# Performance work log

Hardware: AMD Instinct MI355X
Metric: run time of the kernel (lower is better)

Reference implementation:

```python
import jax, jax.numpy as jnp
import numpy as np

SIZE = 512  # context size
T, D1, D2 = 32768, 512, 512
HID = int(SIZE * 1.5)  # 768, units of the 'context_linear' Dense


def setup_inputs() -> dict:
    key = jax.random.key(0)
    ks = jax.random.split(key, 8)
    din = D1 + D2
    return {
        "x1": jax.random.normal(ks[0], (T, D1), jnp.float32),
        "x2": jax.random.normal(ks[1], (T, D2), jnp.float32),
        "context0": jax.random.normal(ks[2], (1, SIZE), jnp.float32) * 0.1,  # tf.Variable init stddev=0.1
        "W_linear": jax.random.normal(ks[3], (din, HID), jnp.float32) * 0.02,
        "b_linear": jnp.zeros((HID,), jnp.float32),
        "W_embed": jax.random.normal(ks[4], (HID, SIZE), jnp.float32) * 0.02,
        "W_rate": jax.random.normal(ks[5], (SIZE, 1), jnp.float32) * 0.02,
        "W_forget": jax.random.normal(ks[6], (SIZE, SIZE), jnp.float32) * 0.02,
    }


def reference(x1, x2, context0, W_linear, b_linear, W_embed, W_rate, W_forget):
    # z = embed(linear(concat(inputs))) : Dense(1.5*size, linear) -> Dense(size, sigmoid, no bias)
    z = jnp.concatenate([x1, x2], axis=-1)                      # [T, D1+D2]
    z = jax.nn.sigmoid((z @ W_linear + b_linear) @ W_embed)     # [T, SIZE]
    # rate gate depends only on z_t, so precompute it in one GEMM
    r = jnp.tanh(z @ W_rate)[:, 0]                              # [T]

    # recurrence: c_t = softmax(c_{t-1} @ Wf) * c_{t-1} + r_t * z_t
    def step(c, zr):
        zt, rt = zr
        f = jax.nn.softmax(c @ W_forget)                        # [SIZE]
        c_new = f * c + rt * zt
        return c_new, c_new

    _, ys = jax.lax.scan(step, context0[0], (z, r))             # ys: [T, SIZE]
    return ys
```

## Files before the change

### kernel.cpp

```cpp
#include <hip/hip_runtime.h>
#include <stdint.h>
#include <stddef.h>


typedef __attribute__((ext_vector_type(8))) short bf16x8;
typedef __attribute__((ext_vector_type(4))) float f32x4;

__device__ __forceinline__ unsigned short f32_to_bf16(float f) {
  union { float f; unsigned u; } v; v.f = f;
  unsigned u = v.u;
  return (unsigned short)((u + 0x7fffu + ((u >> 16) & 1u)) >> 16);
}

__device__ __forceinline__ unsigned char f32_to_e4m3(float f) {
  float a = fabsf(f);
  unsigned char s = (unsigned char)((__float_as_uint(f) >> 24) & 0x80u);
  if (a >= 448.0f) return s | 0x7Eu;
  if (a < 0.015625f) {
    unsigned m = (unsigned)rintf(a * 512.0f);
    return s | (unsigned char)m;
  }
  unsigned u = __float_as_uint(a);
  unsigned r = u + 0x7FFFFu + ((u >> 20) & 1u);
  unsigned e = (r >> 23) - 120u;
  unsigned m = (r >> 20) & 7u;
  if (e >= 16u) return s | 0x7Eu;
  return s | (unsigned char)((e << 3) | m);
}

__device__ __forceinline__ void pack_fp8x8(const float* c, unsigned char* dst) {
  int lo = 0, hi = 0;
  lo = __builtin_amdgcn_cvt_pk_fp8_f32(c[0] * 16.f, c[1] * 16.f, lo, false);
  lo = __builtin_amdgcn_cvt_pk_fp8_f32(c[2] * 16.f, c[3] * 16.f, lo, true);
  hi = __builtin_amdgcn_cvt_pk_fp8_f32(c[4] * 16.f, c[5] * 16.f, hi, false);
  hi = __builtin_amdgcn_cvt_pk_fp8_f32(c[6] * 16.f, c[7] * 16.f, hi, true);
  int2 v; v.x = lo; v.y = hi;
  *(int2*)dst = v;
}

__device__ __forceinline__ void async16(const void* g, void* l) {
  __builtin_amdgcn_global_load_lds(
      (const __attribute__((address_space(1))) unsigned int*)g,
      (__attribute__((address_space(3))) unsigned int*)l, 16, 0, 0);
}

__global__ void k_prep(const float* __restrict__ x1, const float* __restrict__ x2,
                       const float* __restrict__ Wl, const float* __restrict__ We,
                       const float* __restrict__ Wf,
                       unsigned short* __restrict__ Xb,
                       unsigned short* __restrict__ WlT,
                       unsigned short* __restrict__ WeT,
                       unsigned char* __restrict__ Wf8,
                       float* __restrict__ rb) {
  __shared__ float tile[32][33];
  int b = blockIdx.x;
  if (b >= 1440) {
    int id = (b - 1440) * 256 + threadIdx.x;
    int t  = id >> 8;
    int c4 = (id & 255) * 4;
    float4 v;
    if (c4 < 512) v = *(const float4*)(x1 + (size_t)t * 512 + c4);
    else          v = *(const float4*)(x2 + (size_t)t * 512 + (c4 - 512));
    ushort4 o;
    o.x = f32_to_bf16(v.x); o.y = f32_to_bf16(v.y);
    o.z = f32_to_bf16(v.z); o.w = f32_to_bf16(v.w);
    *(ushort4*)(Xb + (size_t)t * 1024 + c4) = o;
    return;
  }
  if (b >= 1408) {
    int idx = (b - 1408) * 256 + threadIdx.x;
    *(float4*)(rb + idx * 4) = float4{0.f, 0.f, 0.f, 0.f};
    return;
  }
  const float* src; int C, tr, tc, mode;
  if (b < 768)       { src = Wl; C = 768; tr = b / 24;  tc = b % 24;  mode = 0; }
  else if (b < 1152) { int j = b - 768;  src = We; C = 512; tr = j / 16; tc = j % 16; mode = 1; }
  else               { int j = b - 1152; src = Wf; C = 512; tr = j / 16; tc = j % 16; mode = 2; }
  const int tx = threadIdx.x & 31, ty = threadIdx.x >> 5;
  const int r0 = tr * 32, c0 = tc * 32;
#pragma unroll
  for (int p = 0; p < 4; ++p)
    tile[ty + p * 8][tx] = src[(size_t)(r0 + ty + p * 8) * C + c0 + tx];
  __syncthreads();
#pragma unroll
  for (int p = 0; p < 4; ++p) {
    int n = c0 + ty + p * 8;
    float v = tile[tx][ty + p * 8];
    if (mode == 0)      WlT[(size_t)n * 1024 + r0 + tx] = f32_to_bf16(v);
    else if (mode == 1) WeT[(size_t)n * 768  + r0 + tx] = f32_to_bf16(v);
    else                Wf8[(size_t)n * 512  + r0 + tx] = f32_to_e4m3(v * 16.0f);
  }
}

template <int MODE>
__global__ void k_gemm_bt(const unsigned short* __restrict__ A,
                          const unsigned short* __restrict__ Bt,
                          const float* __restrict__ aux,
                          unsigned short* __restrict__ Cb,
                          float* __restrict__ Cf,
                          float* __restrict__ rate,
                          int M, int N, int K) {
  __shared__ unsigned short As[128 * 64];
  __shared__ unsigned short Bs[128 * 64];
  const int tid = threadIdx.x;
  const int wv = tid >> 6, lane = tid & 63;
  const int nb = N >> 7;
  const int xcd = blockIdx.x & 7;
  const int s   = blockIdx.x >> 3;
  const int bm  = xcd * (M >> 10) + s / nb;
  const int bn  = s % nb;
  const int wm = wv >> 1, wn = wv & 1;
  f32x4 acc[4][4];
#pragma unroll
  for (int i = 0; i < 4; ++i)
#pragma unroll
    for (int j = 0; j < 4; ++j) acc[i][j] = f32x4{0.f, 0.f, 0.f, 0.f};

  const unsigned short* Ag = A + (size_t)(bm * 128 + wv * 8 + (lane >> 3)) * K + (lane & 7) * 8;
  const unsigned short* Bg = Bt + (size_t)(bn * 128 + wv * 8 + (lane >> 3)) * K + (lane & 7) * 8;
  char* AsW = (char*)As + wv * 1024;
  char* BsW = (char*)Bs + wv * 1024;
  const int lm = lane & 15;
  const int qk = (lane >> 4) * 8;

  for (int k0 = 0; k0 < K; k0 += 64) {
    __syncthreads();
#pragma unroll
    for (int p = 0; p < 4; ++p) {
      async16(Ag + k0 + (size_t)(p * 32) * K, AsW + p * 4096);
      async16(Bg + k0 + (size_t)(p * 32) * K, BsW + p * 4096);
    }
    __syncthreads();
#pragma unroll
    for (int ko = 0; ko < 2; ++ko) {
      bf16x8 af[4], bfr[4];
#pragma unroll
      for (int mt = 0; mt < 4; ++mt)
        af[mt] = *(const bf16x8*)(As + (wm * 64 + mt * 16 + lm) * 64 + ko * 32 + qk);
#pragma unroll
      for (int nt = 0; nt < 4; ++nt)
        bfr[nt] = *(const bf16x8*)(Bs + (wn * 64 + nt * 16 + lm) * 64 + ko * 32 + qk);
#pragma unroll
      for (int mt = 0; mt < 4; ++mt)
#pragma unroll
        for (int nt = 0; nt < 4; ++nt)
          acc[mt][nt] = __builtin_amdgcn_mfma_f32_16x16x32_bf16(af[mt], bfr[nt], acc[mt][nt], 0, 0, 0);
    }
  }

  const int row0 = bm * 128 + wm * 64 + (lane >> 4) * 4;
  const int col0 = bn * 128 + wn * 64 + lm;
  if (MODE == 0) {
#pragma unroll
    for (int mt = 0; mt < 4; ++mt)
#pragma unroll
      for (int nt = 0; nt < 4; ++nt)
#pragma unroll
        for (int rr = 0; rr < 4; ++rr) {
          int row = row0 + mt * 16 + rr;
          int col = col0 + nt * 16;
          Cb[(size_t)row * N + col] = f32_to_bf16(acc[mt][nt][rr] + aux[col]);
        }
  } else {
    float wr[4];
#pragma unroll
    for (int nt = 0; nt < 4; ++nt) wr[nt] = aux[col0 + nt * 16];
#pragma unroll
    for (int mt = 0; mt < 4; ++mt) {
      float rsum[4] = {0.f, 0.f, 0.f, 0.f};
#pragma unroll
      for (int nt = 0; nt < 4; ++nt)
#pragma unroll
        for (int rr = 0; rr < 4; ++rr) {
          int row = row0 + mt * 16 + rr;
          int col = col0 + nt * 16;
          float v = 1.0f / (1.0f + __expf(-acc[mt][nt][rr]));
          Cf[(size_t)row * N + col] = v;
          rsum[rr] += v * wr[nt];
        }
#pragma unroll
      for (int rr = 0; rr < 4; ++rr) {
        float sv = rsum[rr];
        sv += __shfl_xor(sv, 1, 64);
        sv += __shfl_xor(sv, 2, 64);
        sv += __shfl_xor(sv, 4, 64);
        sv += __shfl_xor(sv, 8, 64);
        if (lm == 0) atomicAdd(&rate[row0 + mt * 16 + rr], sv);
      }
    }
  }
}

__global__ __launch_bounds__(1024, 4) void k_recur(
    const unsigned char* __restrict__ Wf8, const float* __restrict__ Z,
    const float* __restrict__ rArr, const float* __restrict__ ctx0,
    float* __restrict__ out) {
  __shared__ unsigned char Cq[16 * 520];
  __shared__ float Lg[16 * 516];

  const int tid = threadIdx.x;
  const int wv = tid >> 6;
  const int lane = tid & 63;
  const int lm = lane & 15;
  const int qk = (lane >> 4) * 8;

  long Bf[2][16];
  const int nbase = wv * 32;
#pragma unroll
  for (int nt = 0; nt < 2; ++nt)
#pragma unroll
    for (int kt = 0; kt < 16; ++kt)
      Bf[nt][kt] = *(const long*)(Wf8 + (size_t)(nbase + nt * 16 + lm) * 512 + kt * 32 + qk);

  const int g = wv;
  const int cg = blockIdx.x * 16 + g;
  const int colBase = lane * 8;
  float c[8];
  if (cg == 0) {
#pragma unroll
    for (int j = 0; j < 8; ++j) c[j] = ctx0[colBase + j];
  } else {
#pragma unroll
    for (int j = 0; j < 8; ++j) c[j] = 0.f;
  }
  pack_fp8x8(c, Cq + g * 520 + colBase);
  __syncthreads();

  for (int s = 0; s < 11; ++s) {
    const int t = cg * 8 - 3 + s;
    float4 za = {0.f, 0.f, 0.f, 0.f}, zb = {0.f, 0.f, 0.f, 0.f};
    float rv = 0.f;
    if (t >= 0) {
      const float4* z4 = (const float4*)(Z + (size_t)t * 512 + colBase);
      za = z4[0]; zb = z4[1];
      rv = rArr[t];
    }

    f32x4 acc0 = {0.f, 0.f, 0.f, 0.f}, acc1 = {0.f, 0.f, 0.f, 0.f};
#pragma unroll
    for (int kt = 0; kt < 16; ++kt) {
      long a = *(const long*)(Cq + lm * 520 + kt * 32 + qk);
      acc0 = __builtin_amdgcn_mfma_f32_16x16x32_fp8_fp8(a, Bf[0][kt], acc0, 0, 0, 0);
      acc1 = __builtin_amdgcn_mfma_f32_16x16x32_fp8_fp8(a, Bf[1][kt], acc1, 0, 0, 0);
    }
#pragma unroll
    for (int rr = 0; rr < 4; ++rr) {
      Lg[((lane >> 4) * 4 + rr) * 516 + nbase + lm]      = acc0[rr];
      Lg[((lane >> 4) * 4 + rr) * 516 + nbase + 16 + lm] = acc1[rr];
    }
    __syncthreads();

    const float ks = 1.4426950408889634f / 256.f;
    const float4* lg4 = (const float4*)(Lg + g * 516 + colBase);
    float4 la = lg4[0], lb = lg4[1];
    float p[8];
    p[0] = exp2f(la.x * ks); p[1] = exp2f(la.y * ks);
    p[2] = exp2f(la.z * ks); p[3] = exp2f(la.w * ks);
    p[4] = exp2f(lb.x * ks); p[5] = exp2f(lb.y * ks);
    p[6] = exp2f(lb.z * ks); p[7] = exp2f(lb.w * ks);
    float sum = ((p[0] + p[1]) + (p[2] + p[3])) + ((p[4] + p[5]) + (p[6] + p[7]));
#pragma unroll
    for (int off = 1; off < 64; off <<= 1) sum += __shfl_xor(sum, off, 64);
    const float inv = __builtin_amdgcn_rcpf(sum);

    if (t >= 0) {
      float xc = fminf(fmaxf(rv, -15.f), 15.f);
      float e2 = __expf(2.f * xc);
      float rt = (e2 - 1.f) * __builtin_amdgcn_rcpf(e2 + 1.f);
      float zz[8] = {za.x, za.y, za.z, za.w, zb.x, zb.y, zb.z, zb.w};
#pragma unroll
      for (int j = 0; j < 8; ++j)
        c[j] = p[j] * inv * c[j] + rt * zz[j];
      if (s >= 3) {
        float4 o0 = {c[0], c[1], c[2], c[3]};
        float4 o1 = {c[4], c[5], c[6], c[7]};
        *(float4*)(out + (size_t)t * 512 + colBase)     = o0;
        *(float4*)(out + (size_t)t * 512 + colBase + 4) = o1;
      }
    }
    pack_fp8x8(c, Cq + g * 520 + colBase);
    __syncthreads();
  }
}

extern "C" void kernel_launch(void* const* d_in, const int* in_sizes, int n_in,
                              void* d_out, int out_size, void* d_ws, size_t ws_size,
                              hipStream_t stream) {
  const float* x1   = (const float*)d_in[0];
  const float* x2   = (const float*)d_in[1];
  const float* ctx0 = (const float*)d_in[2];
  const float* Wl   = (const float*)d_in[3];
  const float* bl   = (const float*)d_in[4];
  const float* We   = (const float*)d_in[5];
  const float* Wr   = (const float*)d_in[6];
  const float* Wf   = (const float*)d_in[7];
  float* out = (float*)d_out;

  char* ws = (char*)d_ws;
  if (ws_size < 120193024u) return;
  unsigned short* Xb  = (unsigned short*)(ws);
  float*          Z32 = (float*)(ws);
  unsigned short* WlT = (unsigned short*)(ws + 67108864);
  unsigned short* WeT = (unsigned short*)(ws + 68681728);
  unsigned char*  Wf8 = (unsigned char*) (ws + 69468160);
  float*          rb  = (float*)         (ws + 69730304);
  unsigned short* H   = (unsigned short*)(ws + 69861376);

  k_prep<<<34208, 256, 0, stream>>>(x1, x2, Wl, We, Wf, Xb, WlT, WeT, Wf8, rb);
  k_gemm_bt<0><<<1536, 256, 0, stream>>>(Xb, WlT, bl, H, nullptr, nullptr, 32768, 768, 1024);
  k_gemm_bt<1><<<1024, 256, 0, stream>>>(H, WeT, Wr, nullptr, Z32, rb, 32768, 512, 768);
  k_recur<<<256, 1024, 0, stream>>>(Wf8, Z32, rb, ctx0, out);
}
```

Before: 330.5 us.

## Replace GEMM with 256x256-tile 8-wave double-buffered swizzled pipeline

Replaces the 128x128 single-buffered bf16 GEMM with a 256x256-tile, 512-thread kernel. It double-buffers 128KB of LDS with async loads issued between MFMA phases, uses XOR-swizzled LDS addressing to avoid bank conflicts, and raises wave priority around the MFMA blocks. The goal is to hide global-load latency and improve data reuse in the two dense layers. In exchange it uses a large LDS footprint and launches far fewer blocks (384 and 256), which may limit occupancy and cause tail imbalance.

```diff
diff --git a/kernel.cpp b/kernel.cpp
--- a/kernel.cpp
+++ b/kernel.cpp
@@ -93,90 +93,140 @@
 }
 
 template <int MODE>
-__global__ void k_gemm_bt(const unsigned short* __restrict__ A,
-                          const unsigned short* __restrict__ Bt,
-                          const float* __restrict__ aux,
-                          unsigned short* __restrict__ Cb,
-                          float* __restrict__ Cf,
-                          float* __restrict__ rate,
-                          int M, int N, int K) {
-  __shared__ unsigned short As[128 * 64];
-  __shared__ unsigned short Bs[128 * 64];
+__global__ __launch_bounds__(512, 2) void k_gemm8(
+    const unsigned short* __restrict__ A, const unsigned short* __restrict__ Bt,
+    const float* __restrict__ aux, unsigned short* __restrict__ Cb,
+    float* __restrict__ Cf, float* __restrict__ rate, int M, int N, int K) {
+  __shared__ char smem[131072];
   const int tid = threadIdx.x;
   const int wv = tid >> 6, lane = tid & 63;
-  const int nb = N >> 7;
-  const int xcd = blockIdx.x & 7;
-  const int s   = blockIdx.x >> 3;
-  const int bm  = xcd * (M >> 10) + s / nb;
-  const int bn  = s % nb;
-  const int wm = wv >> 1, wn = wv & 1;
-  f32x4 acc[4][4];
-#pragma unroll
-  for (int i = 0; i < 4; ++i)
+  const int wm = wv >> 2, wn = wv & 3;
+  const int lm = lane & 15;
+  const int KT = K >> 6;
+  const int NIT = K >> 7;
+  const int nb = N >> 8;
+  const int bpx = gridDim.x >> 3;
+  const int s  = (blockIdx.x & 7) * bpx + (blockIdx.x >> 3);
+  const int bm = s / nb, bn = s % nb;
+
+  const int x0 = wv * 2048 + lane * 16;
+  const int sw = ((lane >> 2) & 3) << 4;
+  const int y0 = x0 ^ sw, y1 = (x0 + 1024) ^ sw;
+  const char* pA0 = (const char*)A  + ((size_t)(bm * 256 + (y0 >> 6)) * K) * 2 + (y0 & 63);
+  const char* pA1 = (const char*)A  + ((size_t)(bm * 256 + (y1 >> 6)) * K) * 2 + (y1 & 63);
+  const char* pB0 = (const char*)Bt + ((size_t)(bn * 256 + (y0 >> 6)) * K) * 2 + (y0 & 63);
+  const char* pB1 = (const char*)Bt + ((size_t)(bn * 256 + (y1 >> 6)) * K) * 2 + (y1 & 63);
+
+  const int cswz = (((lane >> 4) ^ (lane & 3)) << 4);
+
+  f32x4 acc[8][4];
+#pragma unroll
+  for (int i = 0; i < 8; ++i)
 #pragma unroll
     for (int j = 0; j < 4; ++j) acc[i][j] = f32x4{0.f, 0.f, 0.f, 0.f};
-
-  const unsigned short* Ag = A + (size_t)(bm * 128 + wv * 8 + (lane >> 3)) * K + (lane & 7) * 8;
-  const unsigned short* Bg = Bt + (size_t)(bn * 128 + wv * 8 + (lane >> 3)) * K + (lane & 7) * 8;
-  char* AsW = (char*)As + wv * 1024;
-  char* BsW = (char*)Bs + wv * 1024;
-  const int lm = lane & 15;
-  const int qk = (lane >> 4) * 8;
-
-  for (int k0 = 0; k0 < K; k0 += 64) {
-    __syncthreads();
-#pragma unroll
-    for (int p = 0; p < 4; ++p) {
-      async16(Ag + k0 + (size_t)(p * 32) * K, AsW + p * 4096);
-      async16(Bg + k0 + (size_t)(p * 32) * K, BsW + p * 4096);
-    }
-    __syncthreads();
-#pragma unroll
-    for (int ko = 0; ko < 2; ++ko) {
-      bf16x8 af[4], bfr[4];
-#pragma unroll
-      for (int mt = 0; mt < 4; ++mt)
-        af[mt] = *(const bf16x8*)(As + (wm * 64 + mt * 16 + lm) * 64 + ko * 32 + qk);
-#pragma unroll
-      for (int nt = 0; nt < 4; ++nt)
-        bfr[nt] = *(const bf16x8*)(Bs + (wn * 64 + nt * 16 + lm) * 64 + ko * 32 + qk);
-#pragma unroll
-      for (int mt = 0; mt < 4; ++mt)
-#pragma unroll
-        for (int nt = 0; nt < 4; ++nt)
-          acc[mt][nt] = __builtin_amdgcn_mfma_f32_16x16x32_bf16(af[mt], bfr[nt], acc[mt][nt], 0, 0, 0);
-    }
-  }
-
-  const int row0 = bm * 128 + wm * 64 + (lane >> 4) * 4;
-  const int col0 = bn * 128 + wn * 64 + lm;
+  bf16x8 af[4], bf[4];
+
+#define STAGE(SMAT, SKO, SKT) {                                               \
+    size_t koff = (size_t)((SKT) * 64 + (SKO) * 32) * 2;                      \
+    char* d = smem + (((SKT) & 1) * 65536 + (SMAT) * 32768 + (SKO) * 16384 +  \
+                      wv * 2048);                                             \
+    async16(((SMAT) ? pB0 : pA0) + koff, d);                                  \
+    async16(((SMAT) ? pB1 : pA1) + koff, d + 1024); }
+
+#define LDA8(BUF, KO, MQ) {                                                   \
+    const char* ba = smem + ((BUF) * 65536 + (KO) * 16384) +                  \
+                     (wm * 128 + (MQ) * 64 + lm) * 64 + cswz;                 \
+    af[0] = *(const bf16x8*)(ba);        af[1] = *(const bf16x8*)(ba + 1024); \
+    af[2] = *(const bf16x8*)(ba + 2048); af[3] = *(const bf16x8*)(ba + 3072); }
+
+#define LDB8(BUF, KO) {                                                       \
+    const char* bb = smem + ((BUF) * 65536 + 32768 + (KO) * 16384) +          \
+                     (wn * 64 + lm) * 64 + cswz;                              \
+    bf[0] = *(const bf16x8*)(bb);        bf[1] = *(const bf16x8*)(bb + 1024); \
+    bf[2] = *(const bf16x8*)(bb + 2048); bf[3] = *(const bf16x8*)(bb + 3072); }
+
+#define MM16(MQ) {                                                            \
+    _Pragma("unroll") for (int j = 0; j < 4; ++j)                             \
+    _Pragma("unroll") for (int n = 0; n < 4; ++n)                             \
+      acc[(MQ) * 4 + j][n] = __builtin_amdgcn_mfma_f32_16x16x32_bf16(         \
+          af[j], bf[n], acc[(MQ) * 4 + j][n], 0, 0, 0); }
+
+#define PHASE(BUF, KO, MQ, NEWB, SEN, SMAT, SKO, SKT, VM) {                   \
+    if (NEWB) { LDB8(BUF, KO); }                                              \
+    LDA8(BUF, KO, MQ);                                                        \
+    if (SEN) { STAGE(SMAT, SKO, SKT); }                                       \
+    __builtin_amdgcn_s_barrier();                                             \
+    asm volatile("s_waitcnt lgkmcnt(0)" ::: "memory");                        \
+    __builtin_amdgcn_sched_barrier(0);                                        \
+    __builtin_amdgcn_s_setprio(1);                                            \
+    MM16(MQ);                                                                 \
+    __builtin_amdgcn_s_setprio(0);                                            \
+    if ((VM) == 4) { asm volatile("s_waitcnt vmcnt(4)" ::: "memory"); }       \
+    if ((VM) == 0) { asm volatile("s_waitcnt vmcnt(0)" ::: "memory"); }       \
+    __builtin_amdgcn_s_barrier(); }
+
+  STAGE(0, 0, 0) STAGE(1, 0, 0) STAGE(0, 1, 0) STAGE(1, 1, 0)
+  STAGE(0, 0, 1) STAGE(1, 0, 1)
+  asm volatile("s_waitcnt vmcnt(4)" ::: "memory");
+  __builtin_amdgcn_s_barrier();
+
+  for (int it = 0; it < NIT - 1; ++it) {
+    const int t0 = 2 * it;
+    PHASE(0, 0, 0, 1, 1, 0, 1, t0 + 1, -1)
+    PHASE(0, 0, 1, 0, 1, 1, 1, t0 + 1, -1)
+    PHASE(0, 1, 0, 1, 1, 0, 0, t0 + 2, -1)
+    PHASE(0, 1, 1, 0, 1, 1, 0, t0 + 2,  4)
+    PHASE(1, 0, 0, 1, 1, 0, 1, t0 + 2, -1)
+    PHASE(1, 0, 1, 0, 1, 1, 1, t0 + 2, -1)
+    PHASE(1, 1, 0, 1, 1, 0, 0, t0 + 3, -1)
+    PHASE(1, 1, 1, 0, 1, 1, 0, t0 + 3,  4)
+  }
+  {
+    const int t0 = 2 * NIT - 2;
+    PHASE(0, 0, 0, 1, 1, 0, 1, t0 + 1, -1)
+    PHASE(0, 0, 1, 0, 1, 1, 1, t0 + 1, -1)
+    PHASE(0, 1, 0, 1, 0, 0, 0, 0,      -1)
+    PHASE(0, 1, 1, 0, 0, 0, 0, 0,       0)
+    PHASE(1, 0, 0, 1, 0, 0, 0, 0,      -1)
+    PHASE(1, 0, 1, 0, 0, 0, 0, 0,      -1)
+    PHASE(1, 1, 0, 1, 0, 0, 0, 0,      -1)
+    PHASE(1, 1, 1, 0, 0, 0, 0, 0,      -1)
+  }
+#undef STAGE
+#undef LDA8
+#undef LDB8
+#undef MM16
+#undef PHASE
+
+  const int row0 = bm * 256 + wm * 128 + (lane >> 4) * 4;
+  const int col0 = bn * 256 + wn * 64 + lm;
+  float wr[4];
+#pragma unroll
+  for (int n = 0; n < 4; ++n) wr[n] = aux[col0 + n * 16];
   if (MODE == 0) {
 #pragma unroll
-    for (int mt = 0; mt < 4; ++mt)
-#pragma unroll
-      for (int nt = 0; nt < 4; ++nt)
+    for (int m = 0; m < 8; ++m)
+#pragma unroll
+      for (int n = 0; n < 4; ++n)
 #pragma unroll
         for (int rr = 0; rr < 4; ++rr) {
-          int row = row0 + mt * 16 + rr;
-          int col = col0 + nt * 16;
-          Cb[(size_t)row * N + col] = f32_to_bf16(acc[mt][nt][rr] + aux[col]);
+          int row = row0 + m * 16 + rr;
+          int col = col0 + n * 16;
+          Cb[(size_t)row * N + col] = f32_to_bf16(acc[m][n][rr] + wr[n]);
         }
   } else {
-    float wr[4];
-#pragma unroll
-    for (int nt = 0; nt < 4; ++nt) wr[nt] = aux[col0 + nt * 16];
-#pragma unroll
-    for (int mt = 0; mt < 4; ++mt) {
+#pragma unroll
+    for (int m = 0; m < 8; ++m) {
       float rsum[4] = {0.f, 0.f, 0.f, 0.f};
 #pragma unroll
-      for (int nt = 0; nt < 4; ++nt)
+      for (int n = 0; n < 4; ++n)
 #pragma unroll
         for (int rr = 0; rr < 4; ++rr) {
-          int row = row0 + mt * 16 + rr;
-          int col = col0 + nt * 16;
-          float v = 1.0f / (1.0f + __expf(-acc[mt][nt][rr]));
+          int row = row0 + m * 16 + rr;
+          int col = col0 + n * 16;
+          float v = 1.0f / (1.0f + __expf(-acc[m][n][rr]));
           Cf[(size_t)row * N + col] = v;
-          rsum[rr] += v * wr[nt];
+          rsum[rr] += v * wr[n];
         }
 #pragma unroll
       for (int rr = 0; rr < 4; ++rr) {
@@ -185,7 +235,7 @@
         sv += __shfl_xor(sv, 2, 64);
         sv += __shfl_xor(sv, 4, 64);
         sv += __shfl_xor(sv, 8, 64);
-        if (lm == 0) atomicAdd(&rate[row0 + mt * 16 + rr], sv);
+        if (lm == 0) atomicAdd(&rate[row0 + m * 16 + rr], sv);
       }
     }
   }
@@ -307,7 +357,7 @@
   unsigned short* H   = (unsigned short*)(ws + 69861376);
 
   k_prep<<<34208, 256, 0, stream>>>(x1, x2, Wl, We, Wf, Xb, WlT, WeT, Wf8, rb);
-  k_gemm_bt<0><<<1536, 256, 0, stream>>>(Xb, WlT, bl, H, nullptr, nullptr, 32768, 768, 1024);
-  k_gemm_bt<1><<<1024, 256, 0, stream>>>(H, WeT, Wr, nullptr, Z32, rb, 32768, 512, 768);
+  k_gemm8<0><<<384, 512, 0, stream>>>(Xb, WlT, bl, H, nullptr, nullptr, 32768, 768, 1024);
+  k_gemm8<1><<<256, 512, 0, stream>>>(H, WeT, Wr, nullptr, Z32, rb, 32768, 512, 768);
   k_recur<<<256, 1024, 0, stream>>>(Wf8, Z32, rb, ctx0, out);
 }
```

After: 337.4 us. +2.1%, slower.
